# Optimization experiments

Measured on AMD Instinct MI355X. Metric: run time of the kernel, lower is better.

## Reference

```python
import jax, jax.numpy as jnp
import numpy as np

N_NODES = 100000
N_EDGES = 1600000
IN_FEATS = 16
H_FEAT = 64
N_HEADS = 3
N_LAYERS = 8
NUM_CLASSES = 6
HID = H_FEAT * N_HEADS  # 192
NEG_SLOPE = 0.01  # torch F.leaky_relu default


def setup_inputs() -> dict:
    key = jax.random.key(0)
    ks = jax.random.split(key, 10)
    node_feat = jax.random.normal(ks[0], (N_NODES, IN_FEATS), dtype=jnp.float32)
    src = jax.random.randint(ks[1], (N_EDGES,), 0, N_NODES)
    dst = jax.random.randint(ks[2], (N_EDGES,), 0, N_NODES)
    # layer 1 params: per-head fc [H, out, in], attn [H, 2*out]
    W1 = jax.random.normal(ks[3], (N_HEADS, H_FEAT, IN_FEATS), dtype=jnp.float32) * 0.1
    a1 = jax.random.normal(ks[4], (N_HEADS, 2 * H_FEAT), dtype=jnp.float32) * 0.1
    # layers 2..8 params stacked: [L-1, H, out, hid]
    W = jax.random.normal(ks[5], (N_LAYERS - 1, N_HEADS, H_FEAT, HID), dtype=jnp.float32) * 0.1
    a = jax.random.normal(ks[6], (N_LAYERS - 1, N_HEADS, 2 * H_FEAT), dtype=jnp.float32) * 0.1
    fcW = jax.random.normal(ks[7], (NUM_CLASSES, HID), dtype=jnp.float32) * 0.1
    fcb = jnp.zeros((NUM_CLASSES,), dtype=jnp.float32)
    return {"node_feat": node_feat, "src": src, "dst": dst,
            "W1": W1, "a1": a1, "W": W, "a": a, "fcW": fcW, "fcb": fcb}


def _gat_layer(h, src, dst, Wl, al, n_nodes):
    """Multi-head GAT layer (merge='cat'). Wl:[H,O,I], al:[H,2O]."""
    O = Wl.shape[1]
    z = jnp.einsum('ni,hoi->nho', h, Wl)            # [N,H,O]
    a_src, a_dst = al[:, :O], al[:, O:]
    # attn_fc(cat(z_src, z_dst)) decomposed into per-node src/dst scores
    es = jnp.einsum('nho,ho->nh', z, a_src)          # [N,H]
    ed = jnp.einsum('nho,ho->nh', z, a_dst)          # [N,H]
    e = jax.nn.leaky_relu(es[src] + ed[dst], NEG_SLOPE)  # [E,H]
    # segment softmax over incoming edges of each dst node
    m = jax.ops.segment_max(e, dst, num_segments=n_nodes)
    m = jnp.where(jnp.isfinite(m), m, 0.0)
    ex = jnp.exp(e - m[dst])
    den = jax.ops.segment_sum(ex, dst, num_segments=n_nodes)
    alpha = ex / jnp.maximum(den[dst], 1e-9)          # [E,H]
    # scatter-sum aggregation of alpha-weighted source features
    hn = jax.ops.segment_sum(alpha[:, :, None] * z[src], dst, num_segments=n_nodes)  # [N,H,O]
    return hn.reshape(n_nodes, -1)                    # cat heads -> [N,H*O]


def reference(node_feat, src, dst, W1, a1, W, a, fcW, fcb):
    n = node_feat.shape[0]
    h = _gat_layer(node_feat, src, dst, W1, a1, n)
    h = jax.nn.elu(h)
    for l in range(W.shape[0]):
        h = _gat_layer(h, src, dst, W[l], a[l], n)
        h = jax.nn.elu(h)
    return h @ fcW.T + fcb
```

## Files before the change

### kernel.cpp

```cpp
#include <hip/hip_runtime.h>
#include <hip/hip_bf16.h>
#include <hip/hip_fp16.h>
#include <math.h>

#define NN 100000
#define NE 1600000
#define INF_ 16
#define HF 64
#define NH 3
#define HID 192
#define NC 6
#define NEG_SLOPE 0.01f

#define BSH 9
#define NBUCK 196
#define TILE 2048

typedef _Float16 half8 __attribute__((ext_vector_type(8)));
typedef float f32x4 __attribute__((ext_vector_type(4)));


__global__ __launch_bounds__(256) void k_hist(const int* __restrict__ dst, int* __restrict__ deg) {
    int e = blockIdx.x * 256 + threadIdx.x;
    if (e < NE) atomicAdd(&deg[dst[e]], 1);
}

__global__ __launch_bounds__(256) void k_scan1(const int* __restrict__ deg, int* __restrict__ bsum) {
    __shared__ int sc[256];
    int t = threadIdx.x;
    int n = blockIdx.x * 256 + t;
    int v = (n < NN) ? deg[n] : 0;
    sc[t] = v; __syncthreads();
    for (int off = 1; off < 256; off <<= 1) {
        int x = (t >= off) ? sc[t - off] : 0;
        __syncthreads();
        sc[t] += x;
        __syncthreads();
    }
    if (t == 255) bsum[blockIdx.x] = sc[255];
}

__global__ __launch_bounds__(512) void k_scan2(const int* __restrict__ bsum, int* __restrict__ boff, int nb) {
    __shared__ int sc[512];
    int t = threadIdx.x;
    int v = (t < nb) ? bsum[t] : 0;
    sc[t] = v; __syncthreads();
    for (int off = 1; off < 512; off <<= 1) {
        int x = (t >= off) ? sc[t - off] : 0;
        __syncthreads();
        sc[t] += x;
        __syncthreads();
    }
    if (t < nb) boff[t] = sc[t] - v;
}

__global__ __launch_bounds__(256) void k_scan3(const int* __restrict__ deg, const int* __restrict__ boff,
                                               int* __restrict__ row_ptr) {
    __shared__ int sc[256];
    int t = threadIdx.x;
    int n = blockIdx.x * 256 + t;
    int v = (n < NN) ? deg[n] : 0;
    sc[t] = v; __syncthreads();
    for (int off = 1; off < 256; off <<= 1) {
        int x = (t >= off) ? sc[t - off] : 0;
        __syncthreads();
        sc[t] += x;
        __syncthreads();
    }
    if (n < NN) {
        int ex = boff[blockIdx.x] + sc[t] - v;
        row_ptr[n] = ex;
        if (n == NN - 1) row_ptr[NN] = ex + v;
    }
}

__global__ __launch_bounds__(256) void k_binit(const int* __restrict__ row_ptr, int* __restrict__ gcur) {
    int b = threadIdx.x;
    if (b < NBUCK) gcur[b] = row_ptr[min(b << BSH, NN)];
}

__global__ __launch_bounds__(256) void k_bucket(const int* __restrict__ src, const int* __restrict__ dst,
                                                int* __restrict__ gcur, int* __restrict__ staged) {
    __shared__ int cnt[NBUCK], base[NBUCK], cnt2[NBUCK];
    int tid = threadIdx.x;
    int e0 = blockIdx.x * TILE;
    int cntE = min(TILE, NE - e0);
    for (int i = tid; i < NBUCK; i += 256) { cnt[i] = 0; cnt2[i] = 0; }
    __syncthreads();
    int myDst[8], mySrc[8];
#pragma unroll
    for (int k = 0; k < 8; ++k) {
        int idx = tid + k * 256;
        if (idx < cntE) {
            myDst[k] = dst[e0 + idx];
            mySrc[k] = src[e0 + idx];
            atomicAdd(&cnt[myDst[k] >> BSH], 1);
        }
    }
    __syncthreads();
    for (int i = tid; i < NBUCK; i += 256) {
        if (cnt[i] > 0) base[i] = atomicAdd(&gcur[i], cnt[i]);
    }
    __syncthreads();
#pragma unroll
    for (int k = 0; k < 8; ++k) {
        int idx = tid + k * 256;
        if (idx < cntE) {
            int b = myDst[k] >> BSH;
            int r = atomicAdd(&cnt2[b], 1);
            staged[base[b] + r] = ((myDst[k] & 511) << 17) | mySrc[k];
        }
    }
}

__global__ __launch_bounds__(256) void k_bscatter(const int* __restrict__ row_ptr, const int* __restrict__ staged,
                                                  int* __restrict__ colb) {
    __shared__ int cur[512];
    int b = blockIdx.x;
    int n0 = b << BSH;
    int tid = threadIdx.x;
    for (int i = tid; i < 512; i += 256) {
        int n = n0 + i;
        cur[i] = (n < NN) ? row_ptr[n] : 0;
    }
    __syncthreads();
    int beg = row_ptr[n0];
    int end = row_ptr[min(n0 + 512, NN)];
    for (int i = beg + tid; i < end; i += 256) {
        int v = staged[i];
        int d = v >> 17;
        int pos = atomicAdd(&cur[d], 1);
        colb[pos] = (v & 0x1FFFF) * 384;
    }
}


__global__ __launch_bounds__(256) void k_cvtW(const float* __restrict__ W, __half* __restrict__ Wh, int n) {
    int i = blockIdx.x * 256 + threadIdx.x;
    if (i < n) Wh[i] = __float2half(W[i]);
}


__global__ __launch_bounds__(256) void k_prep(const float* __restrict__ W1, const float* __restrict__ a1,
                                              const float* __restrict__ W, const float* __restrict__ a,
                                              float* __restrict__ v0, __half* __restrict__ vh) {
    int bid = blockIdx.x, tid = threadIdx.x;
    if (bid == 0) {
        if (tid < 96) {
            int j = tid >> 4, k = tid & 15;
            int h = j % 3, sd = j / 3;
            float s = 0.f;
            for (int c = 0; c < 64; ++c)
                s += W1[h * 1024 + c * 16 + k] * a1[h * 128 + sd * 64 + c];
            v0[j * 16 + k] = s;
        }
    } else {
        int l = bid - 1;
        if (tid < HID) {
            int k = tid;
            __half* vt = vh + (size_t)l * 16 * HID;
            for (int j = 0; j < 6; ++j) {
                int h = j % 3, sd = j / 3;
                const float* wp = W + (size_t)l * 36864 + h * 12288 + k;
                const float* ap = a + (size_t)l * 384 + h * 128 + sd * 64;
                float s = 0.f;
                for (int c = 0; c < 64; ++c) s += wp[c * 192] * ap[c];
                __half hi = __float2half(s);
                __half lo = __float2half(s - __half2float(hi));
                vt[j * HID + k] = hi;
                vt[(j + 6) * HID + k] = lo;
            }
            for (int j = 12; j < 16; ++j) vt[j * HID + k] = __float2half(0.f);
        }
    }
}


__global__ __launch_bounds__(256) void k_transform1(const float* __restrict__ feat, const float* __restrict__ W1,
                                                    __half* __restrict__ zh) {
    int idx = blockIdx.x * 256 + threadIdx.x;
    if (idx >= NN * HID) return;
    int n = idx / HID;
    int c = idx - n * HID;
    const float* fr = feat + n * INF_;
    const float* wr = W1 + c * INF_;
    float s = 0.f;
#pragma unroll
    for (int i = 0; i < INF_; i += 4) {
        float4 f = *(const float4*)&fr[i];
        float4 w = *(const float4*)&wr[i];
        s += f.x * w.x + f.y * w.y + f.z * w.z + f.w * w.w;
    }
    zh[idx] = __float2half(s);
}


__global__ __launch_bounds__(256) void k_esed1(const float* __restrict__ feat, const float* __restrict__ v0,
                                               float* __restrict__ es, float* __restrict__ ed) {
    __shared__ float sv[96];
    int tid = threadIdx.x;
    if (tid < 96) sv[tid] = v0[tid];
    __syncthreads();
    int n = blockIdx.x * 256 + tid;
    if (n >= NN) return;
    float f[16];
#pragma unroll
    for (int i = 0; i < 16; i += 4) {
        float4 t4 = *(const float4*)&feat[n * 16 + i];
        f[i] = t4.x; f[i + 1] = t4.y; f[i + 2] = t4.z; f[i + 3] = t4.w;
    }
#pragma unroll
    for (int j = 0; j < 6; ++j) {
        float s = 0.f;
#pragma unroll
        for (int k = 0; k < 16; ++k) s += f[k] * sv[j * 16 + k];
        if (j < 3) es[n * 3 + j] = s;
        else ed[n * 3 + (j - 3)] = s;
    }
}


__global__ __launch_bounds__(256) void k_mfma(const __half* __restrict__ Ah, const __half* __restrict__ Whl,
                                              const __half* __restrict__ vhl,
                                              __half* __restrict__ zh, float* __restrict__ es,
                                              float* __restrict__ ed) {
    __shared__ char Bs[73728];
    int tid = threadIdx.x;

#pragma unroll
    for (int i = 0; i < 18; ++i) {
        int idx = tid + i * 256;
        int row = idx / 24;
        int pos = idx - row * 24;
        uint4 v = *(const uint4*)((const char*)Whl + (size_t)idx * 16);
        *(uint4*)(Bs + row * 384 + ((pos * 16) ^ ((row & 7) << 4))) = v;
    }
    __syncthreads();

    int wid = tid >> 6;
    int lane = tid & 63;
    int lrow = lane & 15;
    int lk = lane >> 4;
    int r0 = blockIdx.x * 128 + wid * 32;

    int arow0 = min(r0 + lrow, NN - 1);
    int arow1 = min(r0 + 16 + lrow, NN - 1);
    const __half* ap0 = &Ah[(size_t)arow0 * HID];
    const __half* ap1 = &Ah[(size_t)arow1 * HID];

    f32x4 acc[2][12];
    f32x4 acc13[2];
#pragma unroll
    for (int f = 0; f < 2; ++f) {
        acc13[f] = (f32x4){0.f, 0.f, 0.f, 0.f};
#pragma unroll
        for (int t = 0; t < 12; ++t) acc[f][t] = (f32x4){0.f, 0.f, 0.f, 0.f};
    }

#pragma unroll
    for (int ks = 0; ks < 6; ++ks) {
        half8 a0 = *(const half8*)&ap0[ks * 32 + lk * 8];
        half8 a1 = *(const half8*)&ap1[ks * 32 + lk * 8];
        half8 b13 = *(const half8*)&vhl[lrow * HID + ks * 32 + lk * 8];
        acc13[0] = __builtin_amdgcn_mfma_f32_16x16x32_f16(a0, b13, acc13[0], 0, 0, 0);
        acc13[1] = __builtin_amdgcn_mfma_f32_16x16x32_f16(a1, b13, acc13[1], 0, 0, 0);
#pragma unroll
        for (int t = 0; t < 12; ++t) {
            int brow = t * 16 + lrow;
            half8 bf = *(const half8*)(Bs + brow * 384 + ((ks * 64 + lk * 16) ^ ((brow & 7) << 4)));
            acc[0][t] = __builtin_amdgcn_mfma_f32_16x16x32_f16(a0, bf, acc[0][t], 0, 0, 0);
            acc[1][t] = __builtin_amdgcn_mfma_f32_16x16x32_f16(a1, bf, acc[1][t], 0, 0, 0);
        }
    }

#pragma unroll
    for (int f = 0; f < 2; ++f) {
        int orow0 = r0 + f * 16 + lk * 4;
#pragma unroll
        for (int t = 0; t < 12; ++t) {
#pragma unroll
            for (int g = 0; g < 4; ++g) {
                int row = orow0 + g;
                if (row < NN) zh[(size_t)row * HID + t * 16 + lrow] = __float2half(acc[f][t][g]);
            }
        }
#pragma unroll
        for (int g = 0; g < 4; ++g) {
            float vhi = acc13[f][g];
            float vlo = __shfl(vhi, lane + 6);
            float tot = vhi + vlo;
            int row = orow0 + g;
            if (row < NN) {
                if (lrow < 3) es[row * NH + lrow] = tot;
                else if (lrow < 6) ed[row * NH + (lrow - 3)] = tot;
            }
        }
    }
}


__global__ __launch_bounds__(256) void k_agg(const __half* __restrict__ zh, const int* __restrict__ colb,
                                             const float* __restrict__ es, const float* __restrict__ ed,
                                             const int* __restrict__ row_ptr, __half* __restrict__ h_out) {
    int w = blockIdx.x * 4 + (threadIdx.x >> 6);
    int slot = (threadIdx.x >> 3) & 7;
    int q = threadIdx.x & 7;
    int n = w * 8 + slot;
    int beg = row_ptr[n];
    int deg = row_ptr[n + 1] - beg;

    float3 d3 = *(const float3*)((const char*)ed + n * 12);

    float l0 = 0.f, l1 = 0.f, l2 = 0.f;
    float a0[8], a1[8], a2[8];
#pragma unroll
    for (int k = 0; k < 8; ++k) { a0[k] = 0.f; a1[k] = 0.f; a2[k] = 0.f; }

    const int* cp = colb + beg;
    const char* zb = (const char*)zh + q * 16;

    int soA = 0, soB = 0;
    float3 sA = make_float3(0.f, 0.f, 0.f), sB = sA;
    if (deg > 0) { soA = cp[0]; sA = *(const float3*)((const char*)es + (soA >> 5)); }
    if (deg > 1) { soB = cp[1]; sB = *(const float3*)((const char*)es + (soB >> 5)); }

    int i = 0;
    for (; i + 2 <= deg; i += 2) {
        const char* zpA = zb + soA;
        const char* zpB = zb + soB;
        half8 zA0 = *(const half8*)(zpA);
        half8 zA1 = *(const half8*)(zpA + 128);
        half8 zA2 = *(const half8*)(zpA + 256);
        half8 zB0 = *(const half8*)(zpB);
        half8 zB1 = *(const half8*)(zpB + 128);
        half8 zB2 = *(const half8*)(zpB + 256);
        float xA0 = sA.x + d3.x, xA1 = sA.y + d3.y, xA2 = sA.z + d3.z;
        float xB0 = sB.x + d3.x, xB1 = sB.y + d3.y, xB2 = sB.z + d3.z;
        xA0 = fmaxf(xA0, NEG_SLOPE * xA0); xA1 = fmaxf(xA1, NEG_SLOPE * xA1); xA2 = fmaxf(xA2, NEG_SLOPE * xA2);
        xB0 = fmaxf(xB0, NEG_SLOPE * xB0); xB1 = fmaxf(xB1, NEG_SLOPE * xB1); xB2 = fmaxf(xB2, NEG_SLOPE * xB2);
        float pA0 = __expf(xA0), pA1 = __expf(xA1), pA2 = __expf(xA2);
        float pB0 = __expf(xB0), pB1 = __expf(xB1), pB2 = __expf(xB2);
        if (i + 2 < deg) { soA = cp[i + 2]; sA = *(const float3*)((const char*)es + (soA >> 5)); }
        if (i + 3 < deg) { soB = cp[i + 3]; sB = *(const float3*)((const char*)es + (soB >> 5)); }
        l0 += pA0 + pB0; l1 += pA1 + pB1; l2 += pA2 + pB2;
#pragma unroll
        for (int k = 0; k < 8; ++k) {
            a0[k] += pA0 * (float)zA0[k] + pB0 * (float)zB0[k];
            a1[k] += pA1 * (float)zA1[k] + pB1 * (float)zB1[k];
            a2[k] += pA2 * (float)zA2[k] + pB2 * (float)zB2[k];
        }
    }
    if (i < deg) {
        const char* zpA = zb + soA;
        half8 zA0 = *(const half8*)(zpA);
        half8 zA1 = *(const half8*)(zpA + 128);
        half8 zA2 = *(const half8*)(zpA + 256);
        float xA0 = sA.x + d3.x, xA1 = sA.y + d3.y, xA2 = sA.z + d3.z;
        xA0 = fmaxf(xA0, NEG_SLOPE * xA0); xA1 = fmaxf(xA1, NEG_SLOPE * xA1); xA2 = fmaxf(xA2, NEG_SLOPE * xA2);
        float pA0 = __expf(xA0), pA1 = __expf(xA1), pA2 = __expf(xA2);
        l0 += pA0; l1 += pA1; l2 += pA2;
#pragma unroll
        for (int k = 0; k < 8; ++k) {
            a0[k] += pA0 * (float)zA0[k];
            a1[k] += pA1 * (float)zA1[k];
            a2[k] += pA2 * (float)zA2[k];
        }
    }

    float r0 = 1.f / fmaxf(l0, 1e-9f);
    float r1 = 1.f / fmaxf(l1, 1e-9f);
    float r2 = 1.f / fmaxf(l2, 1e-9f);
    char* ob = (char*)h_out + (size_t)n * 384 + q * 16;
    union { float4 f4; __half2 h2[4]; } u;
#pragma unroll
    for (int k = 0; k < 4; ++k) {
        float x0 = a0[2 * k] * r0, x1 = a0[2 * k + 1] * r0;
        x0 = (x0 > 0.f) ? x0 : (__expf(x0) - 1.f);
        x1 = (x1 > 0.f) ? x1 : (__expf(x1) - 1.f);
        u.h2[k] = __floats2half2_rn(x0, x1);
    }
    *(float4*)ob = u.f4;
#pragma unroll
    for (int k = 0; k < 4; ++k) {
        float x0 = a1[2 * k] * r1, x1 = a1[2 * k + 1] * r1;
        x0 = (x0 > 0.f) ? x0 : (__expf(x0) - 1.f);
        x1 = (x1 > 0.f) ? x1 : (__expf(x1) - 1.f);
        u.h2[k] = __floats2half2_rn(x0, x1);
    }
    *(float4*)(ob + 128) = u.f4;
#pragma unroll
    for (int k = 0; k < 4; ++k) {
        float x0 = a2[2 * k] * r2, x1 = a2[2 * k + 1] * r2;
        x0 = (x0 > 0.f) ? x0 : (__expf(x0) - 1.f);
        x1 = (x1 > 0.f) ? x1 : (__expf(x1) - 1.f);
        u.h2[k] = __floats2half2_rn(x0, x1);
    }
    *(float4*)(ob + 256) = u.f4;
}


__device__ inline float wred_sum(float v) {
#pragma unroll
    for (int o = 32; o; o >>= 1) v += __shfl_xor(v, o);
    return v;
}

__global__ __launch_bounds__(256) void k_fc(const __half* __restrict__ hbuf, const float* __restrict__ fcW,
                                            const float* __restrict__ fcb, float* __restrict__ out) {
    __shared__ float sW[NC * HID];
    __shared__ float sb[NC];
    int tid = threadIdx.x;
    for (int i = tid; i < NC * HID; i += 256) sW[i] = fcW[i];
    if (tid < NC) sb[tid] = fcb[tid];
    __syncthreads();
    int w = tid >> 6;
    int lane = tid & 63;
    int n = blockIdx.x * 4 + w;
    if (n >= NN) return;
    float h0 = __half2float(hbuf[(size_t)n * HID + lane]);
    float h1 = __half2float(hbuf[(size_t)n * HID + 64 + lane]);
    float h2 = __half2float(hbuf[(size_t)n * HID + 128 + lane]);
#pragma unroll
    for (int j = 0; j < NC; ++j) {
        float p = h0 * sW[j * HID + lane] + h1 * sW[j * HID + 64 + lane] + h2 * sW[j * HID + 128 + lane];
        p = wred_sum(p);
        if (lane == 0) out[n * NC + j] = p + sb[j];
    }
}


extern "C" void kernel_launch(void* const* d_in, const int* in_sizes, int n_in,
                              void* d_out, int out_size, void* d_ws, size_t ws_size,
                              hipStream_t stream) {
    const float* node_feat = (const float*)d_in[0];
    const int* src = (const int*)d_in[1];
    const int* dst = (const int*)d_in[2];
    const float* W1 = (const float*)d_in[3];
    const float* a1 = (const float*)d_in[4];
    const float* W = (const float*)d_in[5];
    const float* a = (const float*)d_in[6];
    const float* fcW = (const float*)d_in[7];
    const float* fcb = (const float*)d_in[8];
    float* out = (float*)d_out;

    char* p = (char*)d_ws;
    auto alloc = [&](size_t bytes) {
        void* r = (void*)p;
        p += (bytes + 255) & ~(size_t)255;
        return r;
    };
    int* deg = (int*)alloc(NN * 4);
    int* row_ptr = (int*)alloc((NN + 1) * 4);
    int* bsum = (int*)alloc(512 * 4);
    int* boff = (int*)alloc(512 * 4);
    int* gcur = (int*)alloc(NBUCK * 4);
    int* staged = (int*)alloc((size_t)NE * 4);
    int* colb = (int*)alloc((size_t)NE * 4);
    float* es = (float*)alloc((size_t)NN * NH * 4);
    float* ed = (float*)alloc((size_t)NN * NH * 4);
    __half* zh = (__half*)alloc((size_t)NN * HID * 2);
    __half* hb = (__half*)alloc((size_t)NN * HID * 2);
    const int NWH = 7 * NH * HF * HID;
    __half* Wh = (__half*)alloc((size_t)NWH * 2);
    float* v0 = (float*)alloc(96 * 4);
    __half* vh = (__half*)alloc((size_t)7 * 16 * HID * 2);

    int nb = (NN + 255) / 256;

    hipMemsetAsync(deg, 0, NN * 4, stream);
    k_hist<<<(NE + 255) / 256, 256, 0, stream>>>(dst, deg);
    k_scan1<<<nb, 256, 0, stream>>>(deg, bsum);
    k_scan2<<<1, 512, 0, stream>>>(bsum, boff, nb);
    k_scan3<<<nb, 256, 0, stream>>>(deg, boff, row_ptr);
    k_binit<<<1, 256, 0, stream>>>(row_ptr, gcur);
    k_bucket<<<(NE + TILE - 1) / TILE, 256, 0, stream>>>(src, dst, gcur, staged);
    k_bscatter<<<NBUCK, 256, 0, stream>>>(row_ptr, staged, colb);
    k_cvtW<<<(NWH + 255) / 256, 256, 0, stream>>>(W, Wh, NWH);
    k_prep<<<8, 256, 0, stream>>>(W1, a1, W, a, v0, vh);

    int gAgg = NN / 8 / 4;

    k_transform1<<<(NN * HID + 255) / 256, 256, 0, stream>>>(node_feat, W1, zh);
    k_esed1<<<nb, 256, 0, stream>>>(node_feat, v0, es, ed);
    k_agg<<<gAgg, 256, 0, stream>>>(zh, colb, es, ed, row_ptr, hb);

    for (int l = 0; l < 7; ++l) {
        k_mfma<<<(NN + 127) / 128, 256, 0, stream>>>(hb, Wh + (size_t)l * NH * HF * HID,
                                                     vh + (size_t)l * 16 * HID, zh, es, ed);
        k_agg<<<gAgg, 256, 0, stream>>>(zh, colb, es, ed, row_ptr, hb);
    }

    k_fc<<<(NN + 3) / 4, 256, 0, stream>>>(hb, fcW, fcb, out);
}
```

Before: 1.307 ms.

## Build CSR via bucket histogram and register-tile the first-layer transform

Replaces the per-node degree histogram and three-pass scan with a per-bucket histogram (shared-memory atomics), a single small bucket scan, and per-bucket local counting inside the scatter kernel, which now also writes row_ptr. This drops several kernel launches and the global per-edge atomics on the degree array. The first-layer transform is also restructured so each thread computes a 4-node by 8-channel tile and writes half8 vectors, which reuses feature and weight loads. The cost is heavier shared-memory work in the scatter kernel and more registers per thread in the transform.

```diff
diff --git a/kernel.cpp b/kernel.cpp
--- a/kernel.cpp
+++ b/kernel.cpp
@@ -20,16 +20,24 @@
 typedef float f32x4 __attribute__((ext_vector_type(4)));
 
 
-__global__ __launch_bounds__(256) void k_hist(const int* __restrict__ dst, int* __restrict__ deg) {
-    int e = blockIdx.x * 256 + threadIdx.x;
-    if (e < NE) atomicAdd(&deg[dst[e]], 1);
-}
-
-__global__ __launch_bounds__(256) void k_scan1(const int* __restrict__ deg, int* __restrict__ bsum) {
+__global__ __launch_bounds__(256) void k_bhist(const int* __restrict__ dst, int* __restrict__ bcnt) {
+    __shared__ int c[NBUCK];
+    int tid = threadIdx.x;
+    for (int i = tid; i < NBUCK; i += 256) c[i] = 0;
+    __syncthreads();
+    int e0 = blockIdx.x * TILE;
+    int end = min(e0 + TILE, NE);
+    for (int i = e0 + tid; i < end; i += 256) atomicAdd(&c[dst[i] >> BSH], 1);
+    __syncthreads();
+    for (int i = tid; i < NBUCK; i += 256)
+        if (c[i]) atomicAdd(&bcnt[i], c[i]);
+}
+
+__global__ __launch_bounds__(256) void k_bscan(const int* __restrict__ bcnt, int* __restrict__ bbase,
+                                               int* __restrict__ gcur) {
     __shared__ int sc[256];
     int t = threadIdx.x;
-    int n = blockIdx.x * 256 + t;
-    int v = (n < NN) ? deg[n] : 0;
+    int v = (t < NBUCK) ? bcnt[t] : 0;
     sc[t] = v; __syncthreads();
     for (int off = 1; off < 256; off <<= 1) {
         int x = (t >= off) ? sc[t - off] : 0;
@@ -37,46 +45,11 @@
         sc[t] += x;
         __syncthreads();
     }
-    if (t == 255) bsum[blockIdx.x] = sc[255];
-}
-
-__global__ __launch_bounds__(512) void k_scan2(const int* __restrict__ bsum, int* __restrict__ boff, int nb) {
-    __shared__ int sc[512];
-    int t = threadIdx.x;
-    int v = (t < nb) ? bsum[t] : 0;
-    sc[t] = v; __syncthreads();
-    for (int off = 1; off < 512; off <<= 1) {
-        int x = (t >= off) ? sc[t - off] : 0;
-        __syncthreads();
-        sc[t] += x;
-        __syncthreads();
-    }
-    if (t < nb) boff[t] = sc[t] - v;
-}
-
-__global__ __launch_bounds__(256) void k_scan3(const int* __restrict__ deg, const int* __restrict__ boff,
-                                               int* __restrict__ row_ptr) {
-    __shared__ int sc[256];
-    int t = threadIdx.x;
-    int n = blockIdx.x * 256 + t;
-    int v = (n < NN) ? deg[n] : 0;
-    sc[t] = v; __syncthreads();
-    for (int off = 1; off < 256; off <<= 1) {
-        int x = (t >= off) ? sc[t - off] : 0;
-        __syncthreads();
-        sc[t] += x;
-        __syncthreads();
-    }
-    if (n < NN) {
-        int ex = boff[blockIdx.x] + sc[t] - v;
-        row_ptr[n] = ex;
-        if (n == NN - 1) row_ptr[NN] = ex + v;
-    }
-}
-
-__global__ __launch_bounds__(256) void k_binit(const int* __restrict__ row_ptr, int* __restrict__ gcur) {
-    int b = threadIdx.x;
-    if (b < NBUCK) gcur[b] = row_ptr[min(b << BSH, NN)];
+    if (t < NBUCK) {
+        bbase[t] = sc[t] - v;
+        gcur[t] = sc[t] - v;
+    }
+    if (t == NBUCK - 1) bbase[NBUCK] = sc[t];
 }
 
 __global__ __launch_bounds__(256) void k_bucket(const int* __restrict__ src, const int* __restrict__ dst,
@@ -113,23 +86,41 @@
     }
 }
 
-__global__ __launch_bounds__(256) void k_bscatter(const int* __restrict__ row_ptr, const int* __restrict__ staged,
-                                                  int* __restrict__ colb) {
+__global__ __launch_bounds__(256) void k_bscatter(const int* __restrict__ bbase, const int* __restrict__ staged,
+                                                  int* __restrict__ colb, int* __restrict__ row_ptr) {
+    __shared__ int cnt[512];
     __shared__ int cur[512];
+    __shared__ int ssum[256];
     int b = blockIdx.x;
+    int tid = threadIdx.x;
+    int beg = bbase[b];
+    int end = bbase[b + 1];
+    cnt[2 * tid] = 0; cnt[2 * tid + 1] = 0;
+    __syncthreads();
+    for (int i = beg + tid; i < end; i += 256) atomicAdd(&cnt[staged[i] >> 17], 1);
+    __syncthreads();
+    int a0 = cnt[2 * tid], a1 = cnt[2 * tid + 1];
+    ssum[tid] = a0 + a1;
+    __syncthreads();
+    for (int off = 1; off < 256; off <<= 1) {
+        int x = (tid >= off) ? ssum[tid - off] : 0;
+        __syncthreads();
+        ssum[tid] += x;
+        __syncthreads();
+    }
+    int ex = (tid ? ssum[tid - 1] : 0);
+    int c0 = beg + ex;
+    int c1 = beg + ex + a0;
+    cur[2 * tid] = c0;
+    cur[2 * tid + 1] = c1;
     int n0 = b << BSH;
-    int tid = threadIdx.x;
-    for (int i = tid; i < 512; i += 256) {
-        int n = n0 + i;
-        cur[i] = (n < NN) ? row_ptr[n] : 0;
-    }
-    __syncthreads();
-    int beg = row_ptr[n0];
-    int end = row_ptr[min(n0 + 512, NN)];
+    if (n0 + 2 * tid < NN) row_ptr[n0 + 2 * tid] = c0;
+    if (n0 + 2 * tid + 1 < NN) row_ptr[n0 + 2 * tid + 1] = c1;
+    if (b == NBUCK - 1 && tid == 0) row_ptr[NN] = end;
+    __syncthreads();
     for (int i = beg + tid; i < end; i += 256) {
         int v = staged[i];
-        int d = v >> 17;
-        int pos = atomicAdd(&cur[d], 1);
+        int pos = atomicAdd(&cur[v >> 17], 1);
         colb[pos] = (v & 0x1FFFF) * 384;
     }
 }
@@ -179,19 +170,38 @@
 __global__ __launch_bounds__(256) void k_transform1(const float* __restrict__ feat, const float* __restrict__ W1,
                                                     __half* __restrict__ zh) {
     int idx = blockIdx.x * 256 + threadIdx.x;
-    if (idx >= NN * HID) return;
-    int n = idx / HID;
-    int c = idx - n * HID;
-    const float* fr = feat + n * INF_;
-    const float* wr = W1 + c * INF_;
-    float s = 0.f;
-#pragma unroll
-    for (int i = 0; i < INF_; i += 4) {
-        float4 f = *(const float4*)&fr[i];
-        float4 w = *(const float4*)&wr[i];
-        s += f.x * w.x + f.y * w.y + f.z * w.z + f.w * w.w;
-    }
-    zh[idx] = __float2half(s);
+    if (idx >= (NN / 4) * 24) return;
+    int n4 = idx / 24;
+    int seg = idx - n4 * 24;
+    int nbase = n4 * 4;
+    const float* wr = W1 + seg * 8 * INF_;
+
+    float acc[4][8];
+#pragma unroll
+    for (int j = 0; j < 4; ++j)
+#pragma unroll
+        for (int r = 0; r < 8; ++r) acc[j][r] = 0.f;
+
+#pragma unroll
+    for (int k4 = 0; k4 < 4; ++k4) {
+        float4 f[4], w[8];
+#pragma unroll
+        for (int j = 0; j < 4; ++j) f[j] = *(const float4*)&feat[(nbase + j) * INF_ + k4 * 4];
+#pragma unroll
+        for (int r = 0; r < 8; ++r) w[r] = *(const float4*)&wr[r * INF_ + k4 * 4];
+#pragma unroll
+        for (int j = 0; j < 4; ++j)
+#pragma unroll
+            for (int r = 0; r < 8; ++r)
+                acc[j][r] += f[j].x * w[r].x + f[j].y * w[r].y + f[j].z * w[r].z + f[j].w * w[r].w;
+    }
+#pragma unroll
+    for (int j = 0; j < 4; ++j) {
+        half8 o;
+#pragma unroll
+        for (int r = 0; r < 8; ++r) o[r] = (_Float16)acc[j][r];
+        *(half8*)&zh[(size_t)(nbase + j) * HID + seg * 8] = o;
+    }
 }
 
 
@@ -449,10 +459,9 @@
         p += (bytes + 255) & ~(size_t)255;
         return r;
     };
-    int* deg = (int*)alloc(NN * 4);
     int* row_ptr = (int*)alloc((NN + 1) * 4);
-    int* bsum = (int*)alloc(512 * 4);
-    int* boff = (int*)alloc(512 * 4);
+    int* bcnt = (int*)alloc(NBUCK * 4);
+    int* bbase = (int*)alloc((NBUCK + 1) * 4);
     int* gcur = (int*)alloc(NBUCK * 4);
     int* staged = (int*)alloc((size_t)NE * 4);
     int* colb = (int*)alloc((size_t)NE * 4);
@@ -466,21 +475,20 @@
     __half* vh = (__half*)alloc((size_t)7 * 16 * HID * 2);
 
     int nb = (NN + 255) / 256;
-
-    hipMemsetAsync(deg, 0, NN * 4, stream);
-    k_hist<<<(NE + 255) / 256, 256, 0, stream>>>(dst, deg);
-    k_scan1<<<nb, 256, 0, stream>>>(deg, bsum);
-    k_scan2<<<1, 512, 0, stream>>>(bsum, boff, nb);
-    k_scan3<<<nb, 256, 0, stream>>>(deg, boff, row_ptr);
-    k_binit<<<1, 256, 0, stream>>>(row_ptr, gcur);
-    k_bucket<<<(NE + TILE - 1) / TILE, 256, 0, stream>>>(src, dst, gcur, staged);
-    k_bscatter<<<NBUCK, 256, 0, stream>>>(row_ptr, staged, colb);
+    int gTile = (NE + TILE - 1) / TILE;
+
+    hipMemsetAsync(bcnt, 0, NBUCK * 4, stream);
+    k_bhist<<<gTile, 256, 0, stream>>>(dst, bcnt);
+    k_bscan<<<1, 256, 0, stream>>>(bcnt, bbase, gcur);
+    k_bucket<<<gTile, 256, 0, stream>>>(src, dst, gcur, staged);
+    k_bscatter<<<NBUCK, 256, 0, stream>>>(bbase, staged, colb, row_ptr);
     k_cvtW<<<(NWH + 255) / 256, 256, 0, stream>>>(W, Wh, NWH);
     k_prep<<<8, 256, 0, stream>>>(W1, a1, W, a, v0, vh);
 
     int gAgg = NN / 8 / 4;
-
-    k_transform1<<<(NN * HID + 255) / 256, 256, 0, stream>>>(node_feat, W1, zh);
+    int gT1 = ((NN / 4) * 24 + 255) / 256;
+
+    k_transform1<<<gT1, 256, 0, stream>>>(node_feat, W1, zh);
     k_esed1<<<nb, 256, 0, stream>>>(node_feat, v0, es, ed);
     k_agg<<<gAgg, 256, 0, stream>>>(zh, colb, es, ed, row_ptr, hb);
 
```

Result: faster. 1.206 ms (-7.8%).
